# Performance work log

Measured on AMD Instinct MI355X. Metric: run time of the kernel, lower is better.

## Reference

```python
import jax, jax.numpy as jnp
from jax import lax
import numpy as np

N_SPLITS = 2
N_LEVELS = 3
B, T, C = 32, 1024, 128
HID = 512          # int(input_dim * hidden_size) = 128 * 4
K1, K2 = 5, 3      # first conv kernel_size, second conv kernel=3
N_INTER = 7        # 1 + 2 + 4 interactors in the binary tree
LEAKY_SLOPE = 0.01


def setup_inputs() -> dict:
    key = jax.random.key(0)
    ks = jax.random.split(key, 9)
    w = 0.05  # small init so exp-gating stays well-conditioned
    return {
        "x": jax.random.normal(ks[0], (B, T, C), jnp.float32),
        "mul_w1": jax.random.normal(ks[1], (N_INTER, N_SPLITS, K1, C, HID), jnp.float32) * w,
        "mul_b1": jnp.zeros((N_INTER, N_SPLITS, HID), jnp.float32),
        "mul_w2": jax.random.normal(ks[2], (N_INTER, N_SPLITS, K2, HID, C), jnp.float32) * w,
        "mul_b2": jnp.zeros((N_INTER, N_SPLITS, C), jnp.float32),
        "add_w1": jax.random.normal(ks[3], (N_INTER, N_SPLITS, K1, C, HID), jnp.float32) * w,
        "add_b1": jnp.zeros((N_INTER, N_SPLITS, HID), jnp.float32),
        "add_w2": jax.random.normal(ks[4], (N_INTER, N_SPLITS, K2, HID, C), jnp.float32) * w,
        "add_b2": jnp.zeros((N_INTER, N_SPLITS, C), jnp.float32),
    }


def _leaky(x):
    return jnp.where(x > 0, x, LEAKY_SLOPE * x)


def _causal_conv(x, w, b):
    # x: [B, L, Cin], w: [K, Cin, Cout] (keras WIO layout); 'causal' = left-pad K-1
    k = w.shape[0]
    y = lax.conv_general_dilated(x, w, window_strides=(1,),
                                 padding=[(k - 1, 0)],
                                 dimension_numbers=("NWC", "WIO", "NWC"))
    return y + b


def _conv_seq(x, w1, b1, w2, b2):
    # Conv1D(causal, LeakyReLU 0.01) -> Dropout(identity at inference) -> Conv1D(k=3, causal, tanh)
    h = _leaky(_causal_conv(x, w1, b1))
    return jnp.tanh(_causal_conv(h, w2, b2))


def _interactor(x, idx, p):
    # x: [B, L, C]; strided temporal split into N_SPLITS pieces of length L//N_SPLITS
    splits = [x[:, i::N_SPLITS, :] for i in range(N_SPLITS)]
    scale = N_SPLITS - 1
    mul_list = []
    for i in range(N_SPLITS):
        s = 0.0
        for j in range(N_SPLITS):
            if j != i:
                s = s + _conv_seq(splits[j], p["mul_w1"][idx, i], p["mul_b1"][idx, i],
                                  p["mul_w2"][idx, i], p["mul_b2"][idx, i])
        # prod_j exp(f(x_j)) ** (1/scale) == exp(sum_j f(x_j) / scale)
        mul_list.append(splits[i] * jnp.exp(s / scale))
    out = []
    for i in range(N_SPLITS):
        a = 0.0
        for j in range(N_SPLITS):
            if j != i:
                a = a + _conv_seq(mul_list[j], p["add_w1"][idx, i], p["add_b1"][idx, i],
                                  p["add_w2"][idx, i], p["add_b2"][idx, i])
        a = a / scale
        out.append(mul_list[i] + a if i % 2 == 0 else mul_list[i] - a)
    return out


def reference(x, mul_w1, mul_b1, mul_w2, mul_b2, add_w1, add_b1, add_w2, add_b2):
    p = {"mul_w1": mul_w1, "mul_b1": mul_b1, "mul_w2": mul_w2, "mul_b2": mul_b2,
         "add_w1": add_w1, "add_b1": add_b1, "add_w2": add_w2, "add_b2": add_b2}
    t_in = x.shape[1]
    min_unit = N_SPLITS ** N_LEVELS
    pad = (-t_in) % min_unit  # left zero-pad to a multiple of n_splits**n_levels
    xp = jnp.pad(x, ((0, 0), (pad, 0), (0, 0)))
    seq = [xp]
    idx = 0
    for lvl in range(N_LEVELS):
        nxt = []
        for j in range(N_SPLITS ** lvl):
            nxt += _interactor(seq[j], idx, p)
            idx += 1
        seq = nxt
    # rev_split: recursively concatenate along time with stride `steps`
    while len(seq) > 1:
        steps = len(seq) // N_SPLITS
        seq = [jnp.concatenate([seq[i + s * steps] for s in range(N_SPLITS)], axis=1)
               for i in range(steps)]
    return seq[0][:, -t_in:, :]
```

## Files before the change

kernel.cpp:

```cpp
#include <hip/hip_runtime.h>
#include <hip/hip_bf16.h>
#include <stdint.h>


static constexpr int B_ = 32, T_ = 1024, C_ = 128, HID_ = 512;
static constexpr int K1_ = 5, K2_ = 3;

typedef __attribute__((ext_vector_type(8))) _Float16 half8;
typedef __attribute__((ext_vector_type(4))) float f32x4;

__device__ __forceinline__ unsigned short f2h(float f) {
    _Float16 h = (_Float16)f;
    return __builtin_bit_cast(unsigned short, h);
}

__device__ __forceinline__ void gload16(const void* g, void* l) {
    __builtin_amdgcn_global_load_lds(
        (const __attribute__((address_space(1))) unsigned int*)g,
        (__attribute__((address_space(3))) unsigned int*)l, 16, 0, 0);
}

template<int CIN, int COUT>
__global__ __launch_bounds__(256)
void wprep_k(const float* __restrict__ win, unsigned short* __restrict__ wout,
             int nslabs) {
    constexpr int TA = CIN / 64, TB = COUT / 64;
    int blk = blockIdx.x;
    int tb = blk % TB;
    int ta = (blk / TB) % TA;
    int s  = blk / (TA * TB);
    if (s >= nslabs) return;
    __shared__ float tile[64][65];
    const float* src = win + (size_t)s * CIN * COUT;
    unsigned short* dst = wout + (size_t)s * CIN * COUT;
    int cl = threadIdx.x & 63;
    int rw = threadIdx.x >> 6;
    for (int r = rw; r < 64; r += 4)
        tile[r][cl] = src[(size_t)(ta * 64 + r) * COUT + tb * 64 + cl];
    __syncthreads();
    for (int r = rw; r < 64; r += 4) {
        int co = tb * 64 + r;
        int ci = ta * 64 + cl;
        int ciw = (ci & ~127) | ((ci & 127) ^ ((co & 7) << 3));
        dst[(size_t)co * CIN + ciw] = f2h(tile[cl][r]);
    }
}

__global__ __launch_bounds__(256)
void split_k(const float* __restrict__ cur, unsigned short* __restrict__ outb,
             int Ls) {
    int idx = blockIdx.x * 256 + threadIdx.x;
    int row = idx >> 5;
    int cq  = (idx & 31) << 2;
    int BLs = B_ * Ls;
    int g  = row / BLs;
    int r2 = row - g * BLs;
    int b  = r2 / Ls;
    int u  = r2 - b * Ls;
    int p = g >> 1, i = g & 1;
    const float4 v = *(const float4*)(cur +
        ((size_t)(p * B_ + b) * (2 * Ls) + 2 * u + i) * C_ + cq);
    ushort4 o;
    o.x = f2h(v.x); o.y = f2h(v.y); o.z = f2h(v.z); o.w = f2h(v.w);
    int cqw = cq ^ (((u + 4) & 7) << 3);
    *(ushort4*)(outb + (size_t)row * C_ + cqw) = o;
}

__global__ __launch_bounds__(256, 2)
void conv1_k(const unsigned short* __restrict__ actb,
             const unsigned short* __restrict__ wT,
             const float* __restrict__ bias,
             unsigned short* __restrict__ hid,
             const unsigned short* __restrict__ zp,
             int Ls, int RT, int idxbase) {
    __shared__ unsigned short smemA[132 * 128];
    __shared__ unsigned short smemB[128 * 128];

    const int tid = threadIdx.x;
    const int lane = tid & 63;
    const int w = tid >> 6;
    const int wr = w >> 1, wc = w & 1;

    int blk = blockIdx.x;
    const int ct = blk & 3;
    int t1 = blk >> 2;
    const int rt = t1 % RT;
    const int g  = t1 / RT;
    const int n0 = ct * 128;
    const int rowstart = rt * 128;
    const int b  = rowstart / Ls;
    const int t0 = rowstart - b * Ls;

    const int gin  = g ^ 1;
    const int widx = (idxbase + (g >> 1)) * 2 + (g & 1);

    const char* inb = (const char*)(actb + (size_t)(gin * B_ + b) * Ls * C_);
    const char* wb  = (const char*)(wT + (size_t)widx * (K1_ * HID_ * C_));
    const float* bptr = bias + (size_t)widx * HID_;

    for (int ch = w; ch < 33; ch += 4) {
        int q = ch * 1024 + lane * 16;
        int r = q >> 8;
        int cb = q & 255;
        int t = t0 - 4 + r;
        const char* src = (t >= 0) ? inb + (size_t)t * 256 + cb
                                   : (const char*)zp + cb;
        gload16(src, (char*)smemA + ch * 1024);
    }

    f32x4 acc[4][4];
#pragma unroll
    for (int m = 0; m < 4; ++m)
#pragma unroll
        for (int n = 0; n < 4; ++n) acc[m][n] = (f32x4){0.f, 0.f, 0.f, 0.f};

    for (int kk = 0; kk < K1_; ++kk) {
        if (kk) __syncthreads();
        const char* wt = wb + (size_t)kk * HID_ * C_ * 2;
        for (int ch = w; ch < 32; ch += 4) {
            int q = ch * 1024 + lane * 16;
            int co = q >> 8;
            int cb = q & 255;
            gload16(wt + (size_t)(n0 + co) * 256 + cb, (char*)smemB + ch * 1024);
        }
        asm volatile("s_waitcnt vmcnt(0)" ::: "memory");
        __syncthreads();

#pragma unroll
        for (int ks = 0; ks < 4; ++ks) {
            half8 aF[4], bF[4];
            const int cole = ks * 32 + ((lane >> 4) << 3);
#pragma unroll
            for (int m = 0; m < 4; ++m) {
                int ar = kk + wr * 64 + m * 16 + (lane & 15);
                aF[m] = *(const half8*)(smemA + ar * 128 + (cole ^ ((ar & 7) << 3)));
            }
#pragma unroll
            for (int n = 0; n < 4; ++n) {
                int br = wc * 64 + n * 16 + (lane & 15);
                bF[n] = *(const half8*)(smemB + br * 128 + (cole ^ ((br & 7) << 3)));
            }
#pragma unroll
            for (int m = 0; m < 4; ++m)
#pragma unroll
                for (int n = 0; n < 4; ++n)
                    acc[m][n] = __builtin_amdgcn_mfma_f32_16x16x32_f16(
                        aF[m], bF[n], acc[m][n], 0, 0, 0);
        }
    }

    unsigned short* outp = hid + ((size_t)(g * B_ + b) * Ls + t0) * HID_;
#pragma unroll
    for (int n = 0; n < 4; ++n) {
        int co = n0 + wc * 64 + n * 16 + (lane & 15);
        float bv = bptr[co];
#pragma unroll
        for (int m = 0; m < 4; ++m) {
            int u0 = wr * 64 + m * 16 + ((lane >> 4) << 2);
#pragma unroll
            for (int q = 0; q < 4; ++q) {
                float v = acc[m][n][q] + bv;
                v = (v > 0.f) ? v : 0.01f * v;
                int t = t0 + u0 + q;
                int cow = (co & ~127) | ((co & 127) ^ (((t + 2) & 7) << 3));
                outp[(size_t)(u0 + q) * HID_ + cow] = f2h(v);
            }
        }
    }
}

template<int EPI>
__global__ __launch_bounds__(256, 2)
void conv2_k(const unsigned short* __restrict__ hid,
             const unsigned short* __restrict__ wT,
             const float* __restrict__ bias,
             const float* __restrict__ cur,
             float* __restrict__ mulf,
             unsigned short* __restrict__ actb,
             float* __restrict__ nxt,
             const unsigned short* __restrict__ zp,
             int Ls, int RT, int idxbase) {
    __shared__ unsigned short smemA[66 * 128];
    __shared__ unsigned short smemB[128 * 128];

    const int tid = threadIdx.x;
    const int lane = tid & 63;
    const int w = tid >> 6;
    const int wr = w >> 1, wc = w & 1;

    int blk = blockIdx.x;
    const int rt = blk % RT;
    const int g  = blk / RT;
    const int rowstart = rt * 64;
    const int b  = rowstart / Ls;
    const int t0 = rowstart - b * Ls;
    const int widx = (idxbase + (g >> 1)) * 2 + (g & 1);

    const char* inb = (const char*)(hid + (size_t)(g * B_ + b) * Ls * HID_);
    const char* wb  = (const char*)(wT + (size_t)widx * (K2_ * C_ * HID_));
    const float* bptr = bias + (size_t)widx * C_;

    f32x4 acc[2][4];
#pragma unroll
    for (int m = 0; m < 2; ++m)
#pragma unroll
        for (int n = 0; n < 4; ++n) acc[m][n] = (f32x4){0.f, 0.f, 0.f, 0.f};

    for (int ck = 0; ck < 4; ++ck) {
        if (ck) __syncthreads();
        for (int ch = w; ch < 17; ch += 4) {
            int q = ch * 1024 + lane * 16;
            if (q < 16896) {
                int r = q >> 8;
                int cb = q & 255;
                int t = t0 - 2 + r;
                const char* src = (t >= 0)
                    ? inb + (size_t)t * 1024 + ck * 256 + cb
                    : (const char*)zp + cb;
                gload16(src, (char*)smemA + ch * 1024);
            }
        }
        for (int kk = 0; kk < K2_; ++kk) {
            if (kk) __syncthreads();
            const char* wt = wb + (size_t)kk * C_ * HID_ * 2;
            for (int ch = w; ch < 32; ch += 4) {
                int q = ch * 1024 + lane * 16;
                int co = q >> 8;
                int cb = q & 255;
                gload16(wt + (size_t)co * 1024 + ck * 256 + cb,
                        (char*)smemB + ch * 1024);
            }
            asm volatile("s_waitcnt vmcnt(0)" ::: "memory");
            __syncthreads();

#pragma unroll
            for (int ks = 0; ks < 4; ++ks) {
                half8 aF[2], bF[4];
                const int cole = ks * 32 + ((lane >> 4) << 3);
#pragma unroll
                for (int m = 0; m < 2; ++m) {
                    int ar = kk + wr * 32 + m * 16 + (lane & 15);
                    aF[m] = *(const half8*)(smemA + ar * 128 + (cole ^ ((ar & 7) << 3)));
                }
#pragma unroll
                for (int n = 0; n < 4; ++n) {
                    int br = wc * 64 + n * 16 + (lane & 15);
                    bF[n] = *(const half8*)(smemB + br * 128 + (cole ^ ((br & 7) << 3)));
                }
#pragma unroll
                for (int m = 0; m < 2; ++m)
#pragma unroll
                    for (int n = 0; n < 4; ++n)
                        acc[m][n] = __builtin_amdgcn_mfma_f32_16x16x32_f16(
                            aF[m], bF[n], acc[m][n], 0, 0, 0);
            }
        }
    }

    const size_t rowb = (size_t)(g * B_ + b) * Ls + t0;
    const int p_ = g >> 1, i_ = g & 1;
#pragma unroll
    for (int n = 0; n < 4; ++n) {
        int c = wc * 64 + n * 16 + (lane & 15);
        float bv = bptr[c];
#pragma unroll
        for (int m = 0; m < 2; ++m) {
            int u0 = wr * 32 + m * 16 + ((lane >> 4) << 2);
#pragma unroll
            for (int q = 0; q < 4; ++q) {
                float v = acc[m][n][q] + bv;
                float xc = fminf(fmaxf(v, -15.f), 15.f);
                float e2 = __expf(2.f * xc);
                float th = (e2 - 1.f) / (e2 + 1.f);
                size_t ro = rowb + (size_t)(u0 + q);
                if (EPI == 0) {
                    int u = t0 + u0 + q;
                    float sv = cur[((size_t)(p_ * B_ + b) * (2 * Ls) + 2 * u + i_) * C_ + c];
                    float mv = sv * __expf(th);
                    mulf[ro * C_ + c] = mv;
                    int cw = c ^ (((u + 4) & 7) << 3);
                    actb[ro * C_ + cw] = f2h(mv);
                } else {
                    float mv = mulf[ro * C_ + c];
                    nxt[ro * C_ + c] = (i_ == 0) ? (mv + th) : (mv - th);
                }
            }
        }
    }
}

__global__ __launch_bounds__(256)
void gather_k(const float* __restrict__ src, float* __restrict__ dst) {
    int idx = blockIdx.x * 256 + threadIdx.x;
    int row = idx >> 5;
    int cq  = (idx & 31) << 2;
    int b   = row >> 10;
    int tau = row & 1023;
    int p = ((tau >> 9) & 1) | (((tau >> 8) & 1) << 1) | (((tau >> 7) & 1) << 2);
    int u = tau & 127;
    const float4 v = *(const float4*)(src +
        ((size_t)(p * B_ + b) * 128 + u) * C_ + cq);
    *(float4*)(dst + (size_t)row * C_ + cq) = v;
}

extern "C" void kernel_launch(void* const* d_in, const int* in_sizes, int n_in,
                              void* d_out, int out_size, void* d_ws, size_t ws_size,
                              hipStream_t stream) {
    const float* x   = (const float*)d_in[0];
    const float* mw1 = (const float*)d_in[1];
    const float* mb1 = (const float*)d_in[2];
    const float* mw2 = (const float*)d_in[3];
    const float* mb2 = (const float*)d_in[4];
    const float* aw1 = (const float*)d_in[5];
    const float* ab1 = (const float*)d_in[6];
    const float* aw2 = (const float*)d_in[7];
    const float* ab2 = (const float*)d_in[8];

    char* ws = (char*)d_ws;
    size_t off = 0;
    auto alloc = [&](size_t sz) {
        char* p = ws + off;
        off += (sz + 255) & ~(size_t)255;
        return p;
    };
    unsigned short* zp   = (unsigned short*)alloc(8192);
    unsigned short* w1m  = (unsigned short*)alloc((size_t)14 * 5 * 512 * 128 * 2);
    unsigned short* w1a  = (unsigned short*)alloc((size_t)14 * 5 * 512 * 128 * 2);
    unsigned short* w2m  = (unsigned short*)alloc((size_t)14 * 3 * 128 * 512 * 2);
    unsigned short* w2a  = (unsigned short*)alloc((size_t)14 * 3 * 128 * 512 * 2);
    float* bufA          = (float*)alloc((size_t)4194304 * 4);
    float* bufB          = (float*)alloc((size_t)4194304 * 4);
    unsigned short* actb = (unsigned short*)alloc((size_t)4194304 * 2);
    unsigned short* hidb = (unsigned short*)alloc((size_t)16777216 * 2);
    float* mulf          = (float*)alloc((size_t)4194304 * 4);
    (void)ws_size; (void)n_in; (void)in_sizes; (void)out_size;

    hipMemsetAsync(zp, 0, 8192, stream);

    wprep_k<128, 512><<<1120, 256, 0, stream>>>(mw1, w1m, 70);
    wprep_k<128, 512><<<1120, 256, 0, stream>>>(aw1, w1a, 70);
    wprep_k<512, 128><<<672, 256, 0, stream>>>(mw2, w2m, 42);
    wprep_k<512, 128><<<672, 256, 0, stream>>>(aw2, w2a, 42);

    for (int lvl = 0; lvl < 3; ++lvl) {
        const int P = 1 << lvl;
        const int G = 2 * P;
        const int Ls = (1024 >> lvl) >> 1;
        const int idxbase = P - 1;
        const float* cur = (lvl == 0) ? x : ((lvl == 1) ? bufA : bufB);
        float* nxt = (lvl == 1) ? bufB : bufA;
        const int RT1 = Ls / 4;
        const int RT2 = Ls / 2;

        split_k<<<4096, 256, 0, stream>>>(cur, actb, Ls);
        conv1_k<<<G * RT1 * 4, 256, 0, stream>>>(actb, w1m, mb1, hidb, zp,
                                                 Ls, RT1, idxbase);
        conv2_k<0><<<G * RT2, 256, 0, stream>>>(hidb, w2m, mb2, cur, mulf,
                                                actb, nullptr, zp, Ls, RT2, idxbase);
        conv1_k<<<G * RT1 * 4, 256, 0, stream>>>(actb, w1a, ab1, hidb, zp,
                                                 Ls, RT1, idxbase);
        conv2_k<1><<<G * RT2, 256, 0, stream>>>(hidb, w2a, ab2, nullptr, mulf,
                                                nullptr, nxt, zp, Ls, RT2, idxbase);
    }

    gather_k<<<4096, 256, 0, stream>>>(bufA, (float*)d_out);
}
```

Measured before the change: 376.7 us.

## Fuse split and gather into conv2 epilogues, merge weight prep launches

The add-branch conv2 epilogue now writes the next level's split fp16 activations directly, and at the last level it scatters straight to the output in final time order. This removes the per-level split kernel and the final gather kernel. The two weight-prep launch pairs are each merged into one launch. Conv1 blocks now loop over two 128-column output tiles, halving the grid and reusing the loaded A tile, at the cost of less parallelism and a longer serial loop per block.

```diff
diff --git a/kernel.cpp b/kernel.cpp
--- a/kernel.cpp
+++ b/kernel.cpp
@@ -22,14 +22,18 @@
 
 template<int CIN, int COUT>
 __global__ __launch_bounds__(256)
-void wprep_k(const float* __restrict__ win, unsigned short* __restrict__ wout,
-             int nslabs) {
+void wprep_k(const float* __restrict__ win1, unsigned short* __restrict__ wout1,
+             const float* __restrict__ win2, unsigned short* __restrict__ wout2,
+             int nhalf) {
     constexpr int TA = CIN / 64, TB = COUT / 64;
     int blk = blockIdx.x;
     int tb = blk % TB;
     int ta = (blk / TB) % TA;
     int s  = blk / (TA * TB);
-    if (s >= nslabs) return;
+    const float* win;
+    unsigned short* wout;
+    if (s < nhalf) { win = win1; wout = wout1; }
+    else           { win = win2; wout = wout2; s -= nhalf; }
     __shared__ float tile[64][65];
     const float* src = win + (size_t)s * CIN * COUT;
     unsigned short* dst = wout + (size_t)s * CIN * COUT;
@@ -82,11 +86,10 @@
     const int wr = w >> 1, wc = w & 1;
 
     int blk = blockIdx.x;
-    const int ct = blk & 3;
-    int t1 = blk >> 2;
+    const int ct2 = blk & 1;
+    int t1 = blk >> 1;
     const int rt = t1 % RT;
     const int g  = t1 / RT;
-    const int n0 = ct * 128;
     const int rowstart = rt * 128;
     const int b  = rowstart / Ls;
     const int t0 = rowstart - b * Ls;
@@ -108,62 +111,67 @@
         gload16(src, (char*)smemA + ch * 1024);
     }
 
-    f32x4 acc[4][4];
-#pragma unroll
-    for (int m = 0; m < 4; ++m)
-#pragma unroll
-        for (int n = 0; n < 4; ++n) acc[m][n] = (f32x4){0.f, 0.f, 0.f, 0.f};
-
-    for (int kk = 0; kk < K1_; ++kk) {
-        if (kk) __syncthreads();
-        const char* wt = wb + (size_t)kk * HID_ * C_ * 2;
-        for (int ch = w; ch < 32; ch += 4) {
-            int q = ch * 1024 + lane * 16;
-            int co = q >> 8;
-            int cb = q & 255;
-            gload16(wt + (size_t)(n0 + co) * 256 + cb, (char*)smemB + ch * 1024);
-        }
-        asm volatile("s_waitcnt vmcnt(0)" ::: "memory");
-        __syncthreads();
-
-#pragma unroll
-        for (int ks = 0; ks < 4; ++ks) {
-            half8 aF[4], bF[4];
-            const int cole = ks * 32 + ((lane >> 4) << 3);
+    unsigned short* outp = hid + ((size_t)(g * B_ + b) * Ls + t0) * HID_;
+
+    for (int ctl = 0; ctl < 2; ++ctl) {
+        const int n0 = (ct2 * 2 + ctl) * 128;
+
+        f32x4 acc[4][4];
+#pragma unroll
+        for (int m = 0; m < 4; ++m)
+#pragma unroll
+            for (int n = 0; n < 4; ++n) acc[m][n] = (f32x4){0.f, 0.f, 0.f, 0.f};
+
+        for (int kk = 0; kk < K1_; ++kk) {
+            if (ctl | kk) __syncthreads();
+            const char* wt = wb + (size_t)kk * HID_ * C_ * 2;
+            for (int ch = w; ch < 32; ch += 4) {
+                int q = ch * 1024 + lane * 16;
+                int co = q >> 8;
+                int cb = q & 255;
+                gload16(wt + (size_t)(n0 + co) * 256 + cb, (char*)smemB + ch * 1024);
+            }
+            asm volatile("s_waitcnt vmcnt(0)" ::: "memory");
+            __syncthreads();
+
+#pragma unroll
+            for (int ks = 0; ks < 4; ++ks) {
+                half8 aF[4], bF[4];
+                const int cole = ks * 32 + ((lane >> 4) << 3);
+#pragma unroll
+                for (int m = 0; m < 4; ++m) {
+                    int ar = kk + wr * 64 + m * 16 + (lane & 15);
+                    aF[m] = *(const half8*)(smemA + ar * 128 + (cole ^ ((ar & 7) << 3)));
+                }
+#pragma unroll
+                for (int n = 0; n < 4; ++n) {
+                    int br = wc * 64 + n * 16 + (lane & 15);
+                    bF[n] = *(const half8*)(smemB + br * 128 + (cole ^ ((br & 7) << 3)));
+                }
+#pragma unroll
+                for (int m = 0; m < 4; ++m)
+#pragma unroll
+                    for (int n = 0; n < 4; ++n)
+                        acc[m][n] = __builtin_amdgcn_mfma_f32_16x16x32_f16(
+                            aF[m], bF[n], acc[m][n], 0, 0, 0);
+            }
+        }
+
+#pragma unroll
+        for (int n = 0; n < 4; ++n) {
+            int co = n0 + wc * 64 + n * 16 + (lane & 15);
+            float bv = bptr[co];
 #pragma unroll
             for (int m = 0; m < 4; ++m) {
-                int ar = kk + wr * 64 + m * 16 + (lane & 15);
-                aF[m] = *(const half8*)(smemA + ar * 128 + (cole ^ ((ar & 7) << 3)));
-            }
-#pragma unroll
-            for (int n = 0; n < 4; ++n) {
-                int br = wc * 64 + n * 16 + (lane & 15);
-                bF[n] = *(const half8*)(smemB + br * 128 + (cole ^ ((br & 7) << 3)));
-            }
-#pragma unroll
-            for (int m = 0; m < 4; ++m)
-#pragma unroll
-                for (int n = 0; n < 4; ++n)
-                    acc[m][n] = __builtin_amdgcn_mfma_f32_16x16x32_f16(
-                        aF[m], bF[n], acc[m][n], 0, 0, 0);
-        }
-    }
-
-    unsigned short* outp = hid + ((size_t)(g * B_ + b) * Ls + t0) * HID_;
-#pragma unroll
-    for (int n = 0; n < 4; ++n) {
-        int co = n0 + wc * 64 + n * 16 + (lane & 15);
-        float bv = bptr[co];
-#pragma unroll
-        for (int m = 0; m < 4; ++m) {
-            int u0 = wr * 64 + m * 16 + ((lane >> 4) << 2);
-#pragma unroll
-            for (int q = 0; q < 4; ++q) {
-                float v = acc[m][n][q] + bv;
-                v = (v > 0.f) ? v : 0.01f * v;
-                int t = t0 + u0 + q;
-                int cow = (co & ~127) | ((co & 127) ^ (((t + 2) & 7) << 3));
-                outp[(size_t)(u0 + q) * HID_ + cow] = f2h(v);
+                int u0 = wr * 64 + m * 16 + ((lane >> 4) << 2);
+#pragma unroll
+                for (int q = 0; q < 4; ++q) {
+                    float v = acc[m][n][q] + bv;
+                    v = (v > 0.f) ? v : 0.01f * v;
+                    int t = t0 + u0 + q;
+                    int cow = (co & ~127) | ((co & 127) ^ (((t + 2) & 7) << 3));
+                    outp[(size_t)(u0 + q) * HID_ + cow] = f2h(v);
+                }
             }
         }
     }
@@ -178,6 +186,8 @@
              float* __restrict__ mulf,
              unsigned short* __restrict__ actb,
              float* __restrict__ nxt,
+             unsigned short* __restrict__ actn,
+             float* __restrict__ dout,
              const unsigned short* __restrict__ zp,
              int Ls, int RT, int idxbase) {
     __shared__ unsigned short smemA[66 * 128];
@@ -259,6 +269,7 @@
 
     const size_t rowb = (size_t)(g * B_ + b) * Ls + t0;
     const int p_ = g >> 1, i_ = g & 1;
+    const int Ls2 = Ls >> 1;
 #pragma unroll
     for (int n = 0; n < 4; ++n) {
         int c = wc * 64 + n * 16 + (lane & 15);
@@ -273,8 +284,8 @@
                 float e2 = __expf(2.f * xc);
                 float th = (e2 - 1.f) / (e2 + 1.f);
                 size_t ro = rowb + (size_t)(u0 + q);
+                int u = t0 + u0 + q;
                 if (EPI == 0) {
-                    int u = t0 + u0 + q;
                     float sv = cur[((size_t)(p_ * B_ + b) * (2 * Ls) + 2 * u + i_) * C_ + c];
                     float mv = sv * __expf(th);
                     mulf[ro * C_ + c] = mv;
@@ -282,25 +293,22 @@
                     actb[ro * C_ + cw] = f2h(mv);
                 } else {
                     float mv = mulf[ro * C_ + c];
-                    nxt[ro * C_ + c] = (i_ == 0) ? (mv + th) : (mv - th);
-                }
-            }
-        }
-    }
-}
-
-__global__ __launch_bounds__(256)
-void gather_k(const float* __restrict__ src, float* __restrict__ dst) {
-    int idx = blockIdx.x * 256 + threadIdx.x;
-    int row = idx >> 5;
-    int cq  = (idx & 31) << 2;
-    int b   = row >> 10;
-    int tau = row & 1023;
-    int p = ((tau >> 9) & 1) | (((tau >> 8) & 1) << 1) | (((tau >> 7) & 1) << 2);
-    int u = tau & 127;
-    const float4 v = *(const float4*)(src +
-        ((size_t)(p * B_ + b) * 128 + u) * C_ + cq);
-    *(float4*)(dst + (size_t)row * C_ + cq) = v;
+                    float val = (i_ == 0) ? (mv + th) : (mv - th);
+                    if (EPI == 1) {
+                        nxt[ro * C_ + c] = val;
+                        int gq = g * 2 + (u & 1);
+                        int uq = u >> 1;
+                        int cw = c ^ (((uq + 4) & 7) << 3);
+                        actn[((size_t)(gq * B_ + b) * Ls2 + uq) * C_ + cw] = f2h(val);
+                    } else {
+                        int tau = u | (((g >> 2) & 1) << 7) | (((g >> 1) & 1) << 8)
+                                    | ((g & 1) << 9);
+                        dout[((size_t)b * T_ + tau) * C_ + c] = val;
+                    }
+                }
+            }
+        }
+    }
 }
 
 extern "C" void kernel_launch(void* const* d_in, const int* in_sizes, int n_in,
@@ -337,10 +345,10 @@
 
     hipMemsetAsync(zp, 0, 8192, stream);
 
-    wprep_k<128, 512><<<1120, 256, 0, stream>>>(mw1, w1m, 70);
-    wprep_k<128, 512><<<1120, 256, 0, stream>>>(aw1, w1a, 70);
-    wprep_k<512, 128><<<672, 256, 0, stream>>>(mw2, w2m, 42);
-    wprep_k<512, 128><<<672, 256, 0, stream>>>(aw2, w2a, 42);
+    wprep_k<128, 512><<<2240, 256, 0, stream>>>(mw1, w1m, aw1, w1a, 70);
+    wprep_k<512, 128><<<1344, 256, 0, stream>>>(mw2, w2m, aw2, w2a, 42);
+
+    split_k<<<4096, 256, 0, stream>>>(x, actb, 512);
 
     for (int lvl = 0; lvl < 3; ++lvl) {
         const int P = 1 << lvl;
@@ -352,16 +360,22 @@
         const int RT1 = Ls / 4;
         const int RT2 = Ls / 2;
 
-        split_k<<<4096, 256, 0, stream>>>(cur, actb, Ls);
-        conv1_k<<<G * RT1 * 4, 256, 0, stream>>>(actb, w1m, mb1, hidb, zp,
+        conv1_k<<<G * RT1 * 2, 256, 0, stream>>>(actb, w1m, mb1, hidb, zp,
                                                  Ls, RT1, idxbase);
         conv2_k<0><<<G * RT2, 256, 0, stream>>>(hidb, w2m, mb2, cur, mulf,
-                                                actb, nullptr, zp, Ls, RT2, idxbase);
-        conv1_k<<<G * RT1 * 4, 256, 0, stream>>>(actb, w1a, ab1, hidb, zp,
+                                                actb, nullptr, nullptr, nullptr,
+                                                zp, Ls, RT2, idxbase);
+        conv1_k<<<G * RT1 * 2, 256, 0, stream>>>(actb, w1a, ab1, hidb, zp,
                                                  Ls, RT1, idxbase);
-        conv2_k<1><<<G * RT2, 256, 0, stream>>>(hidb, w2a, ab2, nullptr, mulf,
-                                                nullptr, nxt, zp, Ls, RT2, idxbase);
-    }
-
-    gather_k<<<4096, 256, 0, stream>>>(bufA, (float*)d_out);
-}
+        if (lvl < 2) {
+            conv2_k<1><<<G * RT2, 256, 0, stream>>>(hidb, w2a, ab2, nullptr, mulf,
+                                                    nullptr, nxt, actb, nullptr,
+                                                    zp, Ls, RT2, idxbase);
+        } else {
+            conv2_k<2><<<G * RT2, 256, 0, stream>>>(hidb, w2a, ab2, nullptr, mulf,
+                                                    nullptr, nullptr, nullptr,
+                                                    (float*)d_out,
+                                                    zp, Ls, RT2, idxbase);
+        }
+    }
+}
```

Result: slower. 394.3 us (+4.7%).
